# Kernel tuning notes

Measured on AMD Instinct MI355X. Metric: run time of the kernel, lower is better.

Reference implementation:

```python
import jax, jax.numpy as jnp
from jax import lax
import numpy as np

B, L, E, H = 4, 512, 1024, 128


def setup_inputs() -> dict:
    key = jax.random.key(0)
    k0, k1, k2, k3, k4, k5 = jax.random.split(key, 6)
    s = 1.0 / np.sqrt(E)
    return {
        "rec_emb": jax.random.normal(k0, (B, L, E), jnp.float32),
        "lig_emb": jax.random.normal(k1, (B, L, E), jnp.float32),
        "W1": jax.random.normal(k2, (E, H), jnp.float32) * s,
        "b1": jax.random.normal(k3, (H,), jnp.float32) * 0.01,
        "conv_w": jax.random.normal(k4, (1, H, 2, 2), jnp.float32) * (1.0 / np.sqrt(H * 4)),
        "conv_b": jax.random.normal(k5, (1,), jnp.float32) * 0.01,
    }


def reference(rec_emb, lig_emb, W1, b1, conv_w, conv_b):
    # shared fc: Linear -> ReLU (Dropout is identity in eval mode)
    rec_hid = jax.nn.relu(jnp.einsum("bie,eh->bih", rec_emb, W1) + b1)
    lig_hid = jax.nn.relu(jnp.einsum("bje,eh->bjh", lig_emb, W1) + b1)
    # outer-product bilinear map: bih,bjh->bijh, then tanh
    mat = jnp.tanh(rec_hid[:, :, None, :] * lig_hid[:, None, :, :])
    # permute to NCHW: (b, h, i, j)
    mat = jnp.transpose(mat, (0, 3, 1, 2))
    # Conv2d(H -> 1, kernel=2, padding=1): out spatial = L + 1
    y = lax.conv_general_dilated(
        mat, conv_w, window_strides=(1, 1), padding=[(1, 1), (1, 1)],
        dimension_numbers=("NCHW", "OIHW", "NCHW"),
    ) + conv_b[None, :, None, None]
    # MaxPool2d(kernel=2, stride=2), floor mode
    pooled = lax.reduce_window(
        y, -jnp.inf, lax.max,
        window_dimensions=(1, 1, 2, 2), window_strides=(1, 1, 2, 2),
        padding="VALID",
    )
    # global max over spatial dims -> (b, 1), sigmoid, flatten
    m = jnp.max(pooled, axis=(2, 3))
    return jax.nn.sigmoid(m).reshape(-1)
```

## Files before the change

kernel.cpp:

```cpp
#include <hip/hip_runtime.h>
#include <hip/hip_fp16.h>
#include <math.h>

#define BDIM 4
#define LDIM 512
#define EDIM 1024
#define HDIM 128
#define TILE 32
#define NT   16
#define K2   2.885390081777927f

typedef unsigned short ushort_t;
typedef __attribute__((ext_vector_type(8))) _Float16 half8;
typedef __attribute__((ext_vector_type(4))) float f32x4;

struct __align__(16) H8 { __half2 p[4]; };
union HU { H8 h; half8 v; };

__global__ __launch_bounds__(256) void gemm_direct(
    const float* __restrict__ rec, const float* __restrict__ lig,
    const float* __restrict__ W1, const float* __restrict__ b1,
    ushort_t* __restrict__ hid) {
  const int gw = (int)blockIdx.x * 4 + (threadIdx.x >> 6);
  const int l = threadIdx.x & 63;
  const int strip = gw >> 3;
  const int nidx = gw & 7;
  const int r0 = strip * 16;
  const int m = l & 15, q = l >> 4;
  const float* arow = ((r0 < BDIM * LDIM)
                           ? rec + (size_t)r0 * EDIM
                           : lig + (size_t)(r0 - BDIM * LDIM) * EDIM) +
                      (size_t)m * EDIM + q * 8;
  const int col = nidx * 16 + m;
  const float* wcol = W1 + col;

  f32x4 acc = {0.f, 0.f, 0.f, 0.f};
  for (int blk = 0; blk < 8; ++blk) {
    float4 alo[4], ahi[4];
    float bw[4][8];
#pragma unroll
    for (int j = 0; j < 4; ++j) {
      const int k0 = (blk * 4 + j) * 32 + q * 8;
      alo[j] = *(const float4*)(arow + (blk * 4 + j) * 32);
      ahi[j] = *(const float4*)(arow + (blk * 4 + j) * 32 + 4);
#pragma unroll
      for (int kk = 0; kk < 8; ++kk)
        bw[j][kk] = wcol[(size_t)(k0 + kk) * HDIM];
    }
#pragma unroll
    for (int j = 0; j < 4; ++j) {
      HU au, bu;
      au.h.p[0] = __floats2half2_rn(alo[j].x, alo[j].y);
      au.h.p[1] = __floats2half2_rn(alo[j].z, alo[j].w);
      au.h.p[2] = __floats2half2_rn(ahi[j].x, ahi[j].y);
      au.h.p[3] = __floats2half2_rn(ahi[j].z, ahi[j].w);
      bu.h.p[0] = __floats2half2_rn(bw[j][0], bw[j][1]);
      bu.h.p[1] = __floats2half2_rn(bw[j][2], bw[j][3]);
      bu.h.p[2] = __floats2half2_rn(bw[j][4], bw[j][5]);
      bu.h.p[3] = __floats2half2_rn(bw[j][6], bw[j][7]);
      acc = __builtin_amdgcn_mfma_f32_16x16x32_f16(au.v, bu.v, acc, 0, 0, 0);
    }
  }
  const float scale = (r0 < BDIM * LDIM) ? -K2 : 1.0f;
  const float bias = b1[col];
#pragma unroll
  for (int r = 0; r < 4; ++r) {
    float v = fmaxf(acc[r] + bias, 0.f) * scale;
    ((_Float16*)hid)[(size_t)(r0 + q * 4 + r) * HDIM + col] = (_Float16)v;
  }
}

__global__ __launch_bounds__(256, 5) void bilinear_max(
    const ushort_t* __restrict__ hid, const float* __restrict__ cw,
    const float* __restrict__ cb, float* __restrict__ partial) {
  __shared__ ushort_t rl[33][130];
  __shared__ ushort_t ll[33][130];
  __shared__ ushort_t sl4[33][34][4];
  __shared__ float wred[4];
  __shared__ float wpart[2][4];

  const int t = threadIdx.x;
  const int b = blockIdx.z;
  const int ib = (int)blockIdx.y * TILE - 1;
  const int jb = (int)blockIdx.x * TILE - 1;
  const int w = t >> 6, l = t & 63;
  const int q = l >> 4, c15 = l & 15;

  if (t < HDIM) {
    float4 w4 = *(const float4*)&cw[t * 4];
#pragma unroll
    for (int off = 32; off > 0; off >>= 1) {
      w4.x += __shfl_down(w4.x, off, 64);
      w4.y += __shfl_down(w4.y, off, 64);
      w4.z += __shfl_down(w4.z, off, 64);
      w4.w += __shfl_down(w4.w, off, 64);
    }
    if ((t & 63) == 0) {
      wpart[t >> 6][0] = w4.x; wpart[t >> 6][1] = w4.y;
      wpart[t >> 6][2] = w4.z; wpart[t >> 6][3] = w4.w;
    }
  }

  half8 wf[4];
#pragma unroll
  for (int c = 0; c < 4; ++c) {
#pragma unroll
    for (int j = 0; j < 8; ++j) {
      float v = (c15 < 4) ? cw[(size_t)(c * 32 + q * 8 + j) * 4 + c15] : 0.f;
      wf[c][j] = (_Float16)(-2.f * v);
    }
  }

  H8 z;
  z.p[0] = z.p[1] = z.p[2] = z.p[3] = __floats2half2_rn(0.f, 0.f);
  for (int p = t; p < 66 * 16; p += 256) {
    int r = p >> 4, seg = (p & 15) * 8;
    if (r < 33) {
      int i = ib + r;
      H8 v = z;
      if (i >= 0) v = *(const H8*)&hid[((size_t)(b * LDIM + i)) * HDIM + seg];
      *(H8*)&rl[r][seg] = v;
    } else {
      int j = jb + (r - 33);
      H8 v = z;
      if (j >= 0) v = *(const H8*)&hid[((size_t)((BDIM + b) * LDIM + j)) * HDIM + seg];
      *(H8*)&ll[r - 33][seg] = v;
    }
  }
  __syncthreads();
  const float wsum_v = (c15 < 4) ? (wpart[0][c15] + wpart[1][c15]) : 0.f;

  const __half2 D0 = __float2half2_rn(0.998539f);
  const __half2 D1 = __float2half2_rn(-0.947090f);
  const __half2 D2 = __float2half2_rn(0.676154f);
  const __half2 D3 = __float2half2_rn(-0.228646f);
#define POLYG(U) \
  __hmul2(U, __hfma2(U, __hfma2(U, __hfma2(U, D3, D2), D1), D0))

#pragma unroll
  for (int hf = 0; hf < 2; ++hf) {
    const int jj0 = hf << 4;
    HU lu[4];
#pragma unroll
    for (int c = 0; c < 4; ++c)
      lu[c].v = *(const half8*)&ll[jj0 + c15][c * 32 + q * 8];
    for (int ii8 = 0; ii8 < 8; ++ii8) {
      const int ii = w * 8 + ii8;
      f32x4 acc = {0.f, 0.f, 0.f, 0.f};
#pragma unroll
      for (int c = 0; c < 4; ++c) {
        HU ru, gu;
        ru.v = *(const half8*)&rl[ii][c * 32 + q * 8];
        __half2 u0 = h2exp2(__hmul2(ru.h.p[0], lu[c].h.p[0]));
        __half2 u1 = h2exp2(__hmul2(ru.h.p[1], lu[c].h.p[1]));
        __half2 u2 = h2exp2(__hmul2(ru.h.p[2], lu[c].h.p[2]));
        __half2 u3 = h2exp2(__hmul2(ru.h.p[3], lu[c].h.p[3]));
        gu.h.p[0] = POLYG(u0);
        gu.h.p[1] = POLYG(u1);
        gu.h.p[2] = POLYG(u2);
        gu.h.p[3] = POLYG(u3);
        acc = __builtin_amdgcn_mfma_f32_16x16x32_f16(gu.v, wf[c], acc, 0, 0, 0);
      }
      if (c15 < 4) {
#pragma unroll
        for (int r = 0; r < 4; ++r) {
          _Float16 hv = (_Float16)(wsum_v + acc[r]);
          sl4[ii][jj0 + q * 4 + r][c15] = *(ushort_t*)&hv;
        }
      }
    }
  }
#undef POLYG

  if (t < 65) {
    const int pi = (t < 33) ? t : 32;
    const int qj = (t < 33) ? 32 : (t - 33);
    float4 sa = make_float4(0.f, 0.f, 0.f, 0.f);
    for (int h = 0; h < HDIM; ++h) {
      float rv = (float)(*(const _Float16*)&rl[pi][h]);
      float lv = (float)(*(const _Float16*)&ll[qj][h]);
      float u = __builtin_amdgcn_exp2f(rv * lv);
      float gg = u * fmaf(u, fmaf(u, fmaf(u, -0.228646f, 0.676154f), -0.947090f), 0.998539f);
      float4 w4 = *(const float4*)&cw[h * 4];
      sa.x = fmaf(-2.f * gg, w4.x, sa.x);
      sa.y = fmaf(-2.f * gg, w4.y, sa.y);
      sa.z = fmaf(-2.f * gg, w4.z, sa.z);
      sa.w = fmaf(-2.f * gg, w4.w, sa.w);
    }
#pragma unroll
    for (int k = 0; k < 4; ++k) {
      _Float16 hv = (_Float16)(wpart[0][k] + wpart[1][k] + ((float*)&sa)[k]);
      sl4[pi][qj][k] = *(ushort_t*)&hv;
    }
  }
  __syncthreads();

  float m = -INFINITY;
  const float cbv = cb[0];
  for (int p = t; p < 1024; p += 256) {
    int jj = (p & 31) + 1, iy = (p >> 5) + 1;
    float v = cbv + (float)(*(const _Float16*)&sl4[iy - 1][jj - 1][0])
                  + (float)(*(const _Float16*)&sl4[iy - 1][jj][1])
                  + (float)(*(const _Float16*)&sl4[iy][jj - 1][2])
                  + (float)(*(const _Float16*)&sl4[iy][jj][3]);
    m = fmaxf(m, v);
  }
#pragma unroll
  for (int off = 32; off > 0; off >>= 1) m = fmaxf(m, __shfl_down(m, off, 64));
  if ((t & 63) == 0) wred[t >> 6] = m;
  __syncthreads();
  if (t == 0) {
    float mm = fmaxf(fmaxf(wred[0], wred[1]), fmaxf(wred[2], wred[3]));
    partial[((size_t)b * NT + blockIdx.y) * NT + blockIdx.x] = mm;
  }
}

__global__ __launch_bounds__(64) void finalize(const float* __restrict__ partial,
                                               float* __restrict__ out) {
  const int b = blockIdx.x, t = threadIdx.x;
  float m = -INFINITY;
  for (int p = t; p < NT * NT; p += 64) m = fmaxf(m, partial[b * NT * NT + p]);
#pragma unroll
  for (int off = 32; off > 0; off >>= 1) m = fmaxf(m, __shfl_down(m, off, 64));
  if (t == 0) out[b] = 1.f / (1.f + expf(-m));
}

extern "C" void kernel_launch(void* const* d_in, const int* in_sizes, int n_in,
                              void* d_out, int out_size, void* d_ws, size_t ws_size,
                              hipStream_t stream) {
  const float* rec = (const float*)d_in[0];
  const float* lig = (const float*)d_in[1];
  const float* W1  = (const float*)d_in[2];
  const float* b1  = (const float*)d_in[3];
  const float* cw  = (const float*)d_in[4];
  const float* cb  = (const float*)d_in[5];
  float* out = (float*)d_out;

  ushort_t* hid  = (ushort_t*)d_ws;
  float* partial = (float*)(hid + (size_t)2 * BDIM * LDIM * HDIM);

  gemm_direct<<<dim3(512), 256, 0, stream>>>(rec, lig, W1, b1, hid);
  bilinear_max<<<dim3(NT, NT, BDIM), 256, 0, stream>>>(hid, cw, cb, partial);
  finalize<<<dim3(BDIM), 64, 0, stream>>>(partial, out);
}
```

Measured before the change: 130.7 us.

## Shrink bilinear tiles to 16x16, precompute conv weights in GEMM kernel

Halves the bilinear tile size to 16x16, which gives four times as many blocks with less shared memory each, and raises the occupancy hint to 8. The per-block conv-weight fp16 conversion and the weight-sum reduction move into an extra block of the GEMM kernel, which writes them to workspace. The halo column/row scalar loop is split across four threads per output and combined with shuffles. In exchange, halo overhead per tile grows, since 33 of 289 cells are halo instead of 65 of 1089. The extra block also makes the workspace layout longer.

```diff
diff --git a/kernel.cpp b/kernel.cpp
--- a/kernel.cpp
+++ b/kernel.cpp
@@ -6,8 +6,8 @@
 #define LDIM 512
 #define EDIM 1024
 #define HDIM 128
-#define TILE 32
-#define NT   16
+#define TILE 16
+#define NT   32
 #define K2   2.885390081777927f
 
 typedef unsigned short ushort_t;
@@ -20,7 +20,39 @@
 __global__ __launch_bounds__(256) void gemm_direct(
     const float* __restrict__ rec, const float* __restrict__ lig,
     const float* __restrict__ W1, const float* __restrict__ b1,
-    ushort_t* __restrict__ hid) {
+    const float* __restrict__ cw, ushort_t* __restrict__ hid,
+    ushort_t* __restrict__ wneg, float* __restrict__ wsumg) {
+  if (blockIdx.x == 512) {
+    __shared__ float wp[2][4];
+    const int t = threadIdx.x;
+    if (t < HDIM) {
+      float4 w4 = *(const float4*)&cw[t * 4];
+      _Float16 h0 = (_Float16)(-2.f * w4.x), h1 = (_Float16)(-2.f * w4.y);
+      _Float16 h2 = (_Float16)(-2.f * w4.z), h3 = (_Float16)(-2.f * w4.w);
+      wneg[0 * HDIM + t] = *(ushort_t*)&h0;
+      wneg[1 * HDIM + t] = *(ushort_t*)&h1;
+      wneg[2 * HDIM + t] = *(ushort_t*)&h2;
+      wneg[3 * HDIM + t] = *(ushort_t*)&h3;
+#pragma unroll
+      for (int k = 4; k < 16; ++k) wneg[k * HDIM + t] = 0;
+      float4 ws = w4;
+#pragma unroll
+      for (int off = 32; off > 0; off >>= 1) {
+        ws.x += __shfl_down(ws.x, off, 64);
+        ws.y += __shfl_down(ws.y, off, 64);
+        ws.z += __shfl_down(ws.z, off, 64);
+        ws.w += __shfl_down(ws.w, off, 64);
+      }
+      if ((t & 63) == 0) {
+        wp[t >> 6][0] = ws.x; wp[t >> 6][1] = ws.y;
+        wp[t >> 6][2] = ws.z; wp[t >> 6][3] = ws.w;
+      }
+    }
+    __syncthreads();
+    if (t < 4) wsumg[t] = wp[0][t] + wp[1][t];
+    return;
+  }
+
   const int gw = (int)blockIdx.x * 4 + (threadIdx.x >> 6);
   const int l = threadIdx.x & 63;
   const int strip = gw >> 3;
@@ -70,14 +102,14 @@
   }
 }
 
-__global__ __launch_bounds__(256, 5) void bilinear_max(
-    const ushort_t* __restrict__ hid, const float* __restrict__ cw,
+__global__ __launch_bounds__(256, 8) void bilinear_max(
+    const ushort_t* __restrict__ hid, const ushort_t* __restrict__ wneg,
+    const float* __restrict__ wsumg, const float* __restrict__ cw,
     const float* __restrict__ cb, float* __restrict__ partial) {
-  __shared__ ushort_t rl[33][130];
-  __shared__ ushort_t ll[33][130];
-  __shared__ ushort_t sl4[33][34][4];
+  __shared__ ushort_t rl[17][130];
+  __shared__ ushort_t ll[17][130];
+  __shared__ ushort_t sl4[17][18][4];
   __shared__ float wred[4];
-  __shared__ float wpart[2][4];
 
   const int t = threadIdx.x;
   const int b = blockIdx.z;
@@ -86,49 +118,29 @@
   const int w = t >> 6, l = t & 63;
   const int q = l >> 4, c15 = l & 15;
 
-  if (t < HDIM) {
-    float4 w4 = *(const float4*)&cw[t * 4];
-#pragma unroll
-    for (int off = 32; off > 0; off >>= 1) {
-      w4.x += __shfl_down(w4.x, off, 64);
-      w4.y += __shfl_down(w4.y, off, 64);
-      w4.z += __shfl_down(w4.z, off, 64);
-      w4.w += __shfl_down(w4.w, off, 64);
-    }
-    if ((t & 63) == 0) {
-      wpart[t >> 6][0] = w4.x; wpart[t >> 6][1] = w4.y;
-      wpart[t >> 6][2] = w4.z; wpart[t >> 6][3] = w4.w;
-    }
-  }
-
   half8 wf[4];
 #pragma unroll
-  for (int c = 0; c < 4; ++c) {
-#pragma unroll
-    for (int j = 0; j < 8; ++j) {
-      float v = (c15 < 4) ? cw[(size_t)(c * 32 + q * 8 + j) * 4 + c15] : 0.f;
-      wf[c][j] = (_Float16)(-2.f * v);
-    }
-  }
+  for (int c = 0; c < 4; ++c)
+    wf[c] = *(const half8*)&wneg[c15 * HDIM + c * 32 + q * 8];
+  const float wsum_v = (c15 < 4) ? wsumg[c15] : 0.f;
 
   H8 z;
   z.p[0] = z.p[1] = z.p[2] = z.p[3] = __floats2half2_rn(0.f, 0.f);
-  for (int p = t; p < 66 * 16; p += 256) {
+  for (int p = t; p < 34 * 16; p += 256) {
     int r = p >> 4, seg = (p & 15) * 8;
-    if (r < 33) {
+    if (r < 17) {
       int i = ib + r;
       H8 v = z;
       if (i >= 0) v = *(const H8*)&hid[((size_t)(b * LDIM + i)) * HDIM + seg];
       *(H8*)&rl[r][seg] = v;
     } else {
-      int j = jb + (r - 33);
+      int j = jb + (r - 17);
       H8 v = z;
       if (j >= 0) v = *(const H8*)&hid[((size_t)((BDIM + b) * LDIM + j)) * HDIM + seg];
-      *(H8*)&ll[r - 33][seg] = v;
+      *(H8*)&ll[r - 17][seg] = v;
     }
   }
   __syncthreads();
-  const float wsum_v = (c15 < 4) ? (wpart[0][c15] + wpart[1][c15]) : 0.f;
 
   const __half2 D0 = __float2half2_rn(0.998539f);
   const __half2 D1 = __float2half2_rn(-0.947090f);
@@ -137,46 +149,45 @@
 #define POLYG(U) \
   __hmul2(U, __hfma2(U, __hfma2(U, __hfma2(U, D3, D2), D1), D0))
 
-#pragma unroll
-  for (int hf = 0; hf < 2; ++hf) {
-    const int jj0 = hf << 4;
-    HU lu[4];
-#pragma unroll
-    for (int c = 0; c < 4; ++c)
-      lu[c].v = *(const half8*)&ll[jj0 + c15][c * 32 + q * 8];
-    for (int ii8 = 0; ii8 < 8; ++ii8) {
-      const int ii = w * 8 + ii8;
-      f32x4 acc = {0.f, 0.f, 0.f, 0.f};
-#pragma unroll
-      for (int c = 0; c < 4; ++c) {
-        HU ru, gu;
-        ru.v = *(const half8*)&rl[ii][c * 32 + q * 8];
-        __half2 u0 = h2exp2(__hmul2(ru.h.p[0], lu[c].h.p[0]));
-        __half2 u1 = h2exp2(__hmul2(ru.h.p[1], lu[c].h.p[1]));
-        __half2 u2 = h2exp2(__hmul2(ru.h.p[2], lu[c].h.p[2]));
-        __half2 u3 = h2exp2(__hmul2(ru.h.p[3], lu[c].h.p[3]));
-        gu.h.p[0] = POLYG(u0);
-        gu.h.p[1] = POLYG(u1);
-        gu.h.p[2] = POLYG(u2);
-        gu.h.p[3] = POLYG(u3);
-        acc = __builtin_amdgcn_mfma_f32_16x16x32_f16(gu.v, wf[c], acc, 0, 0, 0);
-      }
-      if (c15 < 4) {
-#pragma unroll
-        for (int r = 0; r < 4; ++r) {
-          _Float16 hv = (_Float16)(wsum_v + acc[r]);
-          sl4[ii][jj0 + q * 4 + r][c15] = *(ushort_t*)&hv;
-        }
+  HU lu[4];
+#pragma unroll
+  for (int c = 0; c < 4; ++c)
+    lu[c].v = *(const half8*)&ll[c15][c * 32 + q * 8];
+#pragma unroll
+  for (int g = 0; g < 4; ++g) {
+    const int ii = w * 4 + g;
+    f32x4 acc = {0.f, 0.f, 0.f, 0.f};
+#pragma unroll
+    for (int c = 0; c < 4; ++c) {
+      HU ru, gu;
+      ru.v = *(const half8*)&rl[ii][c * 32 + q * 8];
+      __half2 u0 = h2exp2(__hmul2(ru.h.p[0], lu[c].h.p[0]));
+      __half2 u1 = h2exp2(__hmul2(ru.h.p[1], lu[c].h.p[1]));
+      __half2 u2 = h2exp2(__hmul2(ru.h.p[2], lu[c].h.p[2]));
+      __half2 u3 = h2exp2(__hmul2(ru.h.p[3], lu[c].h.p[3]));
+      gu.h.p[0] = POLYG(u0);
+      gu.h.p[1] = POLYG(u1);
+      gu.h.p[2] = POLYG(u2);
+      gu.h.p[3] = POLYG(u3);
+      acc = __builtin_amdgcn_mfma_f32_16x16x32_f16(gu.v, wf[c], acc, 0, 0, 0);
+    }
+    if (c15 < 4) {
+#pragma unroll
+      for (int r = 0; r < 4; ++r) {
+        _Float16 hv = (_Float16)(wsum_v + acc[r]);
+        sl4[ii][q * 4 + r][c15] = *(ushort_t*)&hv;
       }
     }
   }
 #undef POLYG
 
-  if (t < 65) {
-    const int pi = (t < 33) ? t : 32;
-    const int qj = (t < 33) ? 32 : (t - 33);
+  if (t < 132) {
+    const int pr = t >> 2;
+    const int hq = (t & 3) * 32;
+    const int pi = (pr < 17) ? pr : 16;
+    const int qj = (pr < 17) ? 16 : (pr - 17);
     float4 sa = make_float4(0.f, 0.f, 0.f, 0.f);
-    for (int h = 0; h < HDIM; ++h) {
+    for (int h = hq; h < hq + 32; ++h) {
       float rv = (float)(*(const _Float16*)&rl[pi][h]);
       float lv = (float)(*(const _Float16*)&ll[qj][h]);
       float u = __builtin_amdgcn_exp2f(rv * lv);
@@ -188,23 +199,27 @@
       sa.w = fmaf(-2.f * gg, w4.w, sa.w);
     }
 #pragma unroll
-    for (int k = 0; k < 4; ++k) {
-      _Float16 hv = (_Float16)(wpart[0][k] + wpart[1][k] + ((float*)&sa)[k]);
-      sl4[pi][qj][k] = *(ushort_t*)&hv;
+    for (int s = 1; s < 4; s <<= 1) {
+      sa.x += __shfl_xor(sa.x, s, 64);
+      sa.y += __shfl_xor(sa.y, s, 64);
+      sa.z += __shfl_xor(sa.z, s, 64);
+      sa.w += __shfl_xor(sa.w, s, 64);
+    }
+    if ((t & 3) == 0) {
+#pragma unroll
+      for (int k = 0; k < 4; ++k) {
+        _Float16 hv = (_Float16)(wsumg[k] + ((float*)&sa)[k]);
+        sl4[pi][qj][k] = *(ushort_t*)&hv;
+      }
     }
   }
   __syncthreads();
 
-  float m = -INFINITY;
-  const float cbv = cb[0];
-  for (int p = t; p < 1024; p += 256) {
-    int jj = (p & 31) + 1, iy = (p >> 5) + 1;
-    float v = cbv + (float)(*(const _Float16*)&sl4[iy - 1][jj - 1][0])
+  const int iy = (t >> 4) + 1, jj = (t & 15) + 1;
+  float m = cb[0] + (float)(*(const _Float16*)&sl4[iy - 1][jj - 1][0])
                   + (float)(*(const _Float16*)&sl4[iy - 1][jj][1])
                   + (float)(*(const _Float16*)&sl4[iy][jj - 1][2])
                   + (float)(*(const _Float16*)&sl4[iy][jj][3]);
-    m = fmaxf(m, v);
-  }
 #pragma unroll
   for (int off = 32; off > 0; off >>= 1) m = fmaxf(m, __shfl_down(m, off, 64));
   if ((t & 63) == 0) wred[t >> 6] = m;
@@ -238,8 +253,10 @@
 
   ushort_t* hid  = (ushort_t*)d_ws;
   float* partial = (float*)(hid + (size_t)2 * BDIM * LDIM * HDIM);
-
-  gemm_direct<<<dim3(512), 256, 0, stream>>>(rec, lig, W1, b1, hid);
-  bilinear_max<<<dim3(NT, NT, BDIM), 256, 0, stream>>>(hid, cw, cb, partial);
+  ushort_t* wneg = (ushort_t*)(partial + NT * NT * BDIM);
+  float* wsumg   = (float*)(wneg + 16 * HDIM);
+
+  gemm_direct<<<dim3(513), 256, 0, stream>>>(rec, lig, W1, b1, cw, hid, wneg, wsumg);
+  bilinear_max<<<dim3(NT, NT, BDIM), 256, 0, stream>>>(hid, wneg, wsumg, cw, cb, partial);
   finalize<<<dim3(BDIM), 64, 0, stream>>>(partial, out);
 }
```

Measured after the change: 142.6 us. 1.09x slower.
